# Optimization experiments

Hardware: AMD Instinct MI355X
Metric: run time of the kernel (lower is better)

Reference implementation:

```python
import jax, jax.numpy as jnp
import numpy as np

B, L, D, H, R = 2, 2048, 1024, 16, 512
HD = D // H  # head dim = 64
EPS = 1e-5


def layernorm(x, g, b):
    mu = jnp.mean(x, axis=-1, keepdims=True)
    var = jnp.mean(jnp.square(x - mu), axis=-1, keepdims=True)
    return (x - mu) * jax.lax.rsqrt(var + EPS) * g + b


def rel_pos_bias(res_pos, size):
    # Equivalent to the torch 'skew' causal_mask: bias[h, i, j] = res_pos[h, i-j]
    # if 0 <= i-j < R else -inf (causal + clipped relative distance).
    d = jnp.arange(size)[:, None] - jnp.arange(size)[None, :]  # (L, L)
    valid = (d >= 0) & (d < res_pos.shape[-1])
    gathered = res_pos[:, jnp.clip(d, 0, res_pos.shape[-1] - 1)]  # (H, L, L)
    return jnp.where(valid, gathered, -jnp.inf)


def setup_inputs() -> dict:
    key = jax.random.key(0)
    ks = jax.random.split(key, 12)
    s = lambda fan: 1.0 / np.sqrt(fan)
    return {
        "x": jax.random.normal(ks[0], (B, L, D), jnp.float32),
        "res_pos": jax.random.normal(ks[1], (H, R), jnp.float32) * 0.02,
        "w_qkv": jax.random.normal(ks[2], (D, 3 * D), jnp.float32) * s(D),
        "b_qkv": jnp.zeros((3 * D,), jnp.float32),
        "w_out": jax.random.normal(ks[3], (D, D), jnp.float32) * s(D),
        "b_out": jnp.zeros((D,), jnp.float32),
        "w1": jax.random.normal(ks[4], (D, 4 * D), jnp.float32) * s(D),
        "b1": jnp.zeros((4 * D,), jnp.float32),
        "w2": jax.random.normal(ks[5], (4 * D, D), jnp.float32) * s(4 * D),
        "b2": jnp.zeros((D,), jnp.float32),
        "ln1_g": jnp.ones((D,), jnp.float32),
        "ln1_b": jnp.zeros((D,), jnp.float32),
        "ln2_g": jnp.ones((D,), jnp.float32),
        "ln2_b": jnp.zeros((D,), jnp.float32),
    }


def reference(x, res_pos, w_qkv, b_qkv, w_out, b_out, w1, b1, w2, b2,
              ln1_g, ln1_b, ln2_g, ln2_b):
    b, l, _ = x.shape
    xn = layernorm(x, ln1_g, ln1_b)  # pre-norm
    qkv = xn @ w_qkv + b_qkv  # (B, L, 3D)
    q, k, v = jnp.split(qkv, 3, axis=-1)
    # (B, H, L, HD)
    q = q.reshape(b, l, H, HD).transpose(0, 2, 1, 3)
    k = k.reshape(b, l, H, HD).transpose(0, 2, 1, 3)
    v = v.reshape(b, l, H, HD).transpose(0, 2, 1, 3)
    scale = 1.0 / np.sqrt(HD)
    scores = jnp.einsum('bhqd,bhkd->bhqk', q, k) * scale
    scores = scores + rel_pos_bias(res_pos, l)[None]  # additive rel-pos causal mask
    attn = jax.nn.softmax(scores, axis=-1)
    ctx = jnp.einsum('bhqk,bhkd->bhqd', attn, v)
    ctx = ctx.transpose(0, 2, 1, 3).reshape(b, l, D)
    x = x + ctx @ w_out + b_out  # residual 1
    h = layernorm(x, ln2_g, ln2_b)
    h = jax.nn.relu(h @ w1 + b1) @ w2 + b2
    return x + h  # residual 2
```

## Files before the change

kernel.cpp:

```cpp
#include <hip/hip_runtime.h>
#include <math.h>

#define B_  2
#define L_  2048
#define D_  1024
#define H_  16
#define R_  512
#define HD_ 64
#define M_  (B_*L_)
#define EPS_ 1e-5f

typedef __attribute__((ext_vector_type(8))) short bf16x8;
typedef __attribute__((ext_vector_type(4))) float f32x4;

__device__ __forceinline__ unsigned short f2bf(float f) {
    unsigned int u = __float_as_uint(f);
    u += 0x7fffu + ((u >> 16) & 1u);
    return (unsigned short)(u >> 16);
}

__device__ __forceinline__ void gl2lds16(const void* g, void* l) {
    __builtin_amdgcn_global_load_lds(
        (const __attribute__((address_space(1))) unsigned int*)g,
        (__attribute__((address_space(3))) unsigned int*)l, 16, 0, 0);
}

__global__ __launch_bounds__(256) void prep_kernel(const float* __restrict__ w_qkv,
                                                   const float* __restrict__ w_out,
                                                   const float* __restrict__ w1,
                                                   const float* __restrict__ w2,
                                                   const float* __restrict__ x,
                                                   const float* __restrict__ ln1_g,
                                                   const float* __restrict__ ln1_b,
                                                   unsigned short* __restrict__ o_qkv,
                                                   unsigned short* __restrict__ o_out,
                                                   unsigned short* __restrict__ o_w1,
                                                   unsigned short* __restrict__ o_w2,
                                                   unsigned short* __restrict__ xn) {
    int id = blockIdx.x;
    int t = threadIdx.x;

    if (id >= 12288) {
        int row = id - 12288;
        const float4* xr = (const float4*)(x + (size_t)row * D_);
        float4 v = xr[t];
        float s  = v.x + v.y + v.z + v.w;
        float ss = v.x*v.x + v.y*v.y + v.z*v.z + v.w*v.w;
        #pragma unroll
        for (int o = 32; o > 0; o >>= 1) {
            s  += __shfl_down(s,  o);
            ss += __shfl_down(ss, o);
        }
        __shared__ float rs[4], rss[4];
        int wave = t >> 6, lane = t & 63;
        if (lane == 0) { rs[wave] = s; rss[wave] = ss; }
        __syncthreads();
        if (t == 0) {
            float a = 0.f, c = 0.f;
            for (int i = 0; i < 4; i++) { a += rs[i]; c += rss[i]; }
            rs[0] = a; rss[0] = c;
        }
        __syncthreads();
        float mean = rs[0] * (1.0f / D_);
        float var  = rss[0] * (1.0f / D_) - mean * mean;
        float inv  = rsqrtf(var + EPS_);
        float4 gv = ((const float4*)ln1_g)[t];
        float4 bv = ((const float4*)ln1_b)[t];
        ushort4 ob;
        ob.x = f2bf((v.x - mean) * inv * gv.x + bv.x);
        ob.y = f2bf((v.y - mean) * inv * gv.y + bv.y);
        ob.z = f2bf((v.z - mean) * inv * gv.z + bv.z);
        ob.w = f2bf((v.w - mean) * inv * gv.w + bv.w);
        ((ushort4*)(xn + (size_t)row * D_))[t] = ob;
        return;
    }

    const float* in; unsigned short* out; int K, N;
    if (id < 3072)      { in = w_qkv; out = o_qkv; K = 1024; N = 3072; }
    else if (id < 4096) { in = w_out; out = o_out; K = 1024; N = 1024; id -= 3072; }
    else if (id < 8192) { in = w1;    out = o_w1;  K = 1024; N = 4096; id -= 4096; }
    else                { in = w2;    out = o_w2;  K = 4096; N = 1024; id -= 8192; }
    int nb = N / 32;
    int bn = (id % nb) * 32, bk = (id / nb) * 32;

    __shared__ float tile[32][33];
    int r = t >> 3, c4 = (t & 7) * 4;
    float4 v = *(const float4*)(in + (size_t)(bk + r) * N + bn + c4);
    tile[r][c4+0] = v.x; tile[r][c4+1] = v.y; tile[r][c4+2] = v.z; tile[r][c4+3] = v.w;
    __syncthreads();
    ushort4 o;
    o.x = f2bf(tile[c4+0][r]);
    o.y = f2bf(tile[c4+1][r]);
    o.z = f2bf(tile[c4+2][r]);
    o.w = f2bf(tile[c4+3][r]);
    *(ushort4*)(out + (size_t)(bn + r) * K + bk + c4) = o;
}

__global__ __launch_bounds__(256) void ln_kernel(const float* __restrict__ x,
                                                 const float* __restrict__ g,
                                                 const float* __restrict__ b,
                                                 unsigned short* __restrict__ out) {
    int row = blockIdx.x;
    int t = threadIdx.x;
    const float4* xr = (const float4*)(x + (size_t)row * D_);
    float4 v = xr[t];
    float s  = v.x + v.y + v.z + v.w;
    float ss = v.x*v.x + v.y*v.y + v.z*v.z + v.w*v.w;
    #pragma unroll
    for (int o = 32; o > 0; o >>= 1) {
        s  += __shfl_down(s,  o);
        ss += __shfl_down(ss, o);
    }
    __shared__ float rs[4], rss[4];
    int wave = t >> 6, lane = t & 63;
    if (lane == 0) { rs[wave] = s; rss[wave] = ss; }
    __syncthreads();
    if (t == 0) {
        float a = 0.f, c = 0.f;
        for (int i = 0; i < 4; i++) { a += rs[i]; c += rss[i]; }
        rs[0] = a; rss[0] = c;
    }
    __syncthreads();
    float mean = rs[0] * (1.0f / D_);
    float var  = rss[0] * (1.0f / D_) - mean * mean;
    float inv  = rsqrtf(var + EPS_);
    float4 gv = ((const float4*)g)[t];
    float4 bv = ((const float4*)b)[t];
    ushort4 ob;
    ob.x = f2bf((v.x - mean) * inv * gv.x + bv.x);
    ob.y = f2bf((v.y - mean) * inv * gv.y + bv.y);
    ob.z = f2bf((v.z - mean) * inv * gv.z + bv.z);
    ob.w = f2bf((v.w - mean) * inv * gv.w + bv.w);
    ((ushort4*)(out + (size_t)row * D_))[t] = ob;
}

template<int BM, int KSPLIT, int RELU, int OUT_BF16>
__global__ __launch_bounds__(256) void gemm_mfma(const unsigned short* __restrict__ A,
                                                 const unsigned short* __restrict__ Wt,
                                                 const float* __restrict__ bias,
                                                 const float* __restrict__ res,
                                                 void* __restrict__ Cout,
                                                 int M, int N, int K) {
    constexpr int BN = 128;
    constexpr int BK = KSPLIT * 32;
    constexpr int TM = BM / 32;
    __shared__ __align__(16) unsigned short As[KSPLIT * BM * 32];
    __shared__ __align__(16) unsigned short Bs[KSPLIT * BN * 32];
    int t = threadIdx.x;
    int wave = t >> 6, lane = t & 63;
    int q = lane >> 4, cl = lane & 15;
    int bm = blockIdx.x * BM, bn = blockIdx.y * BN;
    int wm = (wave >> 1) * (BM / 2);
    int wn = (wave & 1) * 64;

    int sm  = t >> 2;
    int scx = t & 3;
    int ssrc = (scx ^ (sm & 3)) * 8;
    int sdst = scx * 8;

    int qa = (q ^ (cl & 3)) * 8;

    f32x4 acc[TM][4] = {};

    for (int kt = 0; kt < K; kt += BK) {
        __syncthreads();
        #pragma unroll
        for (int hh = 0; hh < KSPLIT; hh++) {
            #pragma unroll
            for (int s = 0; s < BM / 64; s++)
                gl2lds16(A + (size_t)(bm + s*64 + sm) * K + kt + hh*32 + ssrc,
                         &As[hh * BM * 32 + (s*64 + sm) * 32 + sdst]);
            #pragma unroll
            for (int s = 0; s < 2; s++)
                gl2lds16(Wt + (size_t)(bn + s*64 + sm) * K + kt + hh*32 + ssrc,
                         &Bs[hh * BN * 32 + (s*64 + sm) * 32 + sdst]);
        }
        __syncthreads();

        #pragma unroll
        for (int hh = 0; hh < KSPLIT; hh++) {
            bf16x8 af[TM], bfr[4];
            #pragma unroll
            for (int i = 0; i < TM; i++)
                af[i] = *(const bf16x8*)&As[hh * BM * 32 + (wm + i*16 + cl) * 32 + qa];
            #pragma unroll
            for (int j = 0; j < 4; j++)
                bfr[j] = *(const bf16x8*)&Bs[hh * BN * 32 + (wn + j*16 + cl) * 32 + qa];
            #pragma unroll
            for (int i = 0; i < TM; i++)
                #pragma unroll
                for (int j = 0; j < 4; j++)
                    acc[i][j] = __builtin_amdgcn_mfma_f32_16x16x32_bf16(
                                    af[i], bfr[j], acc[i][j], 0, 0, 0);
        }
    }

    #pragma unroll
    for (int i = 0; i < TM; i++) {
        #pragma unroll
        for (int j = 0; j < 4; j++) {
            #pragma unroll
            for (int r = 0; r < 4; r++) {
                int row = bm + wm + i*16 + q*4 + r;
                int col = bn + wn + j*16 + cl;
                float v = acc[i][j][r] + bias[col];
                if (RELU) v = fmaxf(v, 0.0f);
                if (res)  v += res[(size_t)row * N + col];
                if (OUT_BF16)
                    ((unsigned short*)Cout)[(size_t)row * N + col] = f2bf(v);
                else
                    ((float*)Cout)[(size_t)row * N + col] = v;
            }
        }
    }
}

#define AP_ 80
__global__ __launch_bounds__(256) void attn_mfma_kernel(const unsigned short* __restrict__ qkv,
                                                        const float* __restrict__ res_pos,
                                                        unsigned short* __restrict__ ctx) {
    int q0 = blockIdx.x * 128;
    int h  = blockIdx.y;
    int b  = blockIdx.z;
    int t  = threadIdx.x;
    int w  = t >> 6, lane = t & 63;
    int quad = lane >> 4, cl = lane & 15;

    __shared__ __align__(16) unsigned short sQP[128 * AP_];
    __shared__ __align__(16) unsigned short sK [64 * AP_];
    __shared__ __align__(16) unsigned short sVt[64 * AP_];
    __shared__ float sBias[R_];

    const int bL = b * L_;
    const unsigned short* base = qkv + (size_t)bL * 3072;

    #pragma unroll
    for (int c = t; c < 1024; c += 256) {
        int row = c >> 3, off = (c & 7) * 8;
        uint4 v = *(const uint4*)(base + (size_t)(q0 + row) * 3072 + h * HD_ + off);
        *(uint4*)&sQP[row * AP_ + off] = v;
    }
    sBias[t]       = res_pos[h * R_ + t]       - 20.0f;
    sBias[t + 256] = res_pos[h * R_ + t + 256] - 20.0f;
    __syncthreads();

    bf16x8 qf[2][2];
    #pragma unroll
    for (int i = 0; i < 2; i++) {
        qf[i][0] = *(const bf16x8*)&sQP[(w*32 + i*16 + cl) * AP_ + quad*8];
        qf[i][1] = *(const bf16x8*)&sQP[(w*32 + i*16 + cl) * AP_ + 32 + quad*8];
    }

    f32x4 accO[2][4] = {};
    float l_r[2][4] = {};

    int klo = q0 - (R_ - 1); if (klo < 0) klo = 0;
    int kt0 = klo & ~63;
    const float scale = 0.125f;

    for (int k0 = kt0; k0 <= q0 + 64; k0 += 64) {
        __syncthreads();
        #pragma unroll
        for (int c = t; c < 512; c += 256) {
            int row = c >> 3, off = (c & 7) * 8;
            uint4 v = *(const uint4*)(base + (size_t)(k0 + row) * 3072 + D_ + h * HD_ + off);
            *(uint4*)&sK[row * AP_ + off] = v;
        }
        {
            int c2 = t & 31, dg = t >> 5;
            int cl_ = c2 & 15, jb = (c2 >> 4) * 2;
            int ka = jb * 16 + cl_;
            const unsigned short* va = base + (size_t)(k0 + ka) * 3072 + 2*D_ + h * HD_ + dg*8;
            uint4 a4 = *(const uint4*)va;
            uint4 b4 = *(const uint4*)(va + (size_t)16 * 3072);
            const unsigned short* pa = (const unsigned short*)&a4;
            const unsigned short* pb = (const unsigned short*)&b4;
            #pragma unroll
            for (int i = 0; i < 8; i++) {
                unsigned int packed = (unsigned int)pa[i] | ((unsigned int)pb[i] << 16);
                *(unsigned int*)&sVt[(dg*8 + i) * AP_ + 4*cl_ + jb] = packed;
            }
        }
        __syncthreads();

        f32x4 sacc[2][4] = {};
        #pragma unroll
        for (int j = 0; j < 4; j++) {
            bf16x8 kf0 = *(const bf16x8*)&sK[(j*16 + cl) * AP_ + quad*8];
            bf16x8 kf1 = *(const bf16x8*)&sK[(j*16 + cl) * AP_ + 32 + quad*8];
            #pragma unroll
            for (int i = 0; i < 2; i++) {
                sacc[i][j] = __builtin_amdgcn_mfma_f32_16x16x32_bf16(qf[i][0], kf0, sacc[i][j], 0, 0, 0);
                sacc[i][j] = __builtin_amdgcn_mfma_f32_16x16x32_bf16(qf[i][1], kf1, sacc[i][j], 0, 0, 0);
            }
        }

        #pragma unroll
        for (int i = 0; i < 2; i++) {
            #pragma unroll
            for (int r = 0; r < 4; r++) {
                int qrow = q0 + w*32 + i*16 + quad*4 + r;
                unsigned short pk[4];
                float lacc = 0.f;
                #pragma unroll
                for (int j = 0; j < 4; j++) {
                    int key = k0 + j*16 + cl;
                    int diff = qrow - key;
                    bool valid = ((unsigned)diff) < (unsigned)R_;
                    int dc = valid ? diff : 0;
                    float p = valid ? __expf(fmaf(sacc[i][j][r], scale, sBias[dc])) : 0.f;
                    lacc += p;
                    pk[j] = f2bf(p);
                }
                l_r[i][r] += lacc;
                unsigned int lo = (unsigned int)pk[0] | ((unsigned int)pk[1] << 16);
                unsigned int hi = (unsigned int)pk[2] | ((unsigned int)pk[3] << 16);
                uint2 pv; pv.x = lo; pv.y = hi;
                *(uint2*)&sQP[(w*32 + i*16 + quad*4 + r) * AP_ + 4*cl] = pv;
            }
        }
        __syncthreads();

        bf16x8 pf[2][2];
        #pragma unroll
        for (int i = 0; i < 2; i++) {
            pf[i][0] = *(const bf16x8*)&sQP[(w*32 + i*16 + cl) * AP_ + quad*8];
            pf[i][1] = *(const bf16x8*)&sQP[(w*32 + i*16 + cl) * AP_ + 32 + quad*8];
        }
        #pragma unroll
        for (int j = 0; j < 4; j++) {
            bf16x8 vf0 = *(const bf16x8*)&sVt[(j*16 + cl) * AP_ + quad*8];
            bf16x8 vf1 = *(const bf16x8*)&sVt[(j*16 + cl) * AP_ + 32 + quad*8];
            #pragma unroll
            for (int i = 0; i < 2; i++) {
                accO[i][j] = __builtin_amdgcn_mfma_f32_16x16x32_bf16(pf[i][0], vf0, accO[i][j], 0, 0, 0);
                accO[i][j] = __builtin_amdgcn_mfma_f32_16x16x32_bf16(pf[i][1], vf1, accO[i][j], 0, 0, 0);
            }
        }
    }

    #pragma unroll
    for (int i = 0; i < 2; i++) {
        #pragma unroll
        for (int r = 0; r < 4; r++) {
            float l = l_r[i][r];
            #pragma unroll
            for (int o = 8; o > 0; o >>= 1) l += __shfl_xor(l, o);
            float inv = 1.0f / l;
            int row = bL + q0 + w*32 + i*16 + quad*4 + r;
            #pragma unroll
            for (int j = 0; j < 4; j++)
                ctx[(size_t)row * D_ + h * HD_ + j*16 + cl] = f2bf(accO[i][j][r] * inv);
        }
    }
}

extern "C" void kernel_launch(void* const* d_in, const int* in_sizes, int n_in,
                              void* d_out, int out_size, void* d_ws, size_t ws_size,
                              hipStream_t stream) {
    const float* x      = (const float*)d_in[0];
    const float* res_pos= (const float*)d_in[1];
    const float* w_qkv  = (const float*)d_in[2];
    const float* b_qkv  = (const float*)d_in[3];
    const float* w_out  = (const float*)d_in[4];
    const float* b_out  = (const float*)d_in[5];
    const float* w1     = (const float*)d_in[6];
    const float* b1     = (const float*)d_in[7];
    const float* w2     = (const float*)d_in[8];
    const float* b2     = (const float*)d_in[9];
    const float* ln1_g  = (const float*)d_in[10];
    const float* ln1_b  = (const float*)d_in[11];
    const float* ln2_g  = (const float*)d_in[12];
    const float* ln2_b  = (const float*)d_in[13];
    float* out = (float*)d_out;
    char* ws = (char*)d_ws;

    unsigned short* act_bf = (unsigned short*)ws;
    unsigned short* wqkvT  = (unsigned short*)(ws + ((size_t)8  << 20));
    unsigned short* woutT  = (unsigned short*)(ws + ((size_t)14 << 20));
    unsigned short* w1T    = (unsigned short*)(ws + ((size_t)16 << 20));
    unsigned short* w2T    = (unsigned short*)(ws + ((size_t)24 << 20));
    unsigned short* qkv_bf = (unsigned short*)(ws + ((size_t)32 << 20));
    unsigned short* h1_bf  = (unsigned short*)(ws + ((size_t)32 << 20));

    prep_kernel<<<16384, 256, 0, stream>>>(w_qkv, w_out, w1, w2,
                                           x, ln1_g, ln1_b,
                                           wqkvT, woutT, w1T, w2T, act_bf);
    gemm_mfma<64,2,0,1><<<dim3(M_/64, 3072/128), 256, 0, stream>>>(
        act_bf, wqkvT, b_qkv, nullptr, qkv_bf, M_, 3072, 1024);
    attn_mfma_kernel<<<dim3(L_/128, H_, B_), 256, 0, stream>>>(qkv_bf, res_pos, act_bf);
    gemm_mfma<64,4,0,0><<<dim3(M_/64, 1024/128), 256, 0, stream>>>(
        act_bf, woutT, b_out, x, out, M_, 1024, 1024);
    ln_kernel<<<M_, 256, 0, stream>>>(out, ln2_g, ln2_b, act_bf);
    gemm_mfma<64,2,1,1><<<dim3(M_/64, 4096/128), 256, 0, stream>>>(
        act_bf, w1T, b1, nullptr, h1_bf, M_, 4096, 1024);
    gemm_mfma<64,4,0,0><<<dim3(M_/64, 1024/128), 256, 0, stream>>>(
        h1_bf, w2T, b2, out, out, M_, 1024, 4096);
}
```

Baseline: 349.3 us.

## Fuse all stages into one persistent kernel with software grid barriers

New measurement: 712.9 us. 104% more time.

```diff
diff --git a/kernel.cpp b/kernel.cpp
--- a/kernel.cpp
+++ b/kernel.cpp
@@ -9,6 +9,8 @@
 #define HD_ 64
 #define M_  (B_*L_)
 #define EPS_ 1e-5f
+#define GRID_ 512
+#define MAGIC_ 0x13572468u
 
 typedef __attribute__((ext_vector_type(8))) short bf16x8;
 typedef __attribute__((ext_vector_type(4))) float f32x4;
@@ -25,24 +27,336 @@
         (__attribute__((address_space(3))) unsigned int*)l, 16, 0, 0);
 }
 
-__global__ __launch_bounds__(256) void prep_kernel(const float* __restrict__ w_qkv,
-                                                   const float* __restrict__ w_out,
-                                                   const float* __restrict__ w1,
-                                                   const float* __restrict__ w2,
-                                                   const float* __restrict__ x,
-                                                   const float* __restrict__ ln1_g,
-                                                   const float* __restrict__ ln1_b,
-                                                   unsigned short* __restrict__ o_qkv,
-                                                   unsigned short* __restrict__ o_out,
-                                                   unsigned short* __restrict__ o_w1,
-                                                   unsigned short* __restrict__ o_w2,
-                                                   unsigned short* __restrict__ xn) {
-    int id = blockIdx.x;
+__device__ __forceinline__ void grid_barrier(unsigned* bar, int blk) {
+    __syncthreads();
+    if (threadIdx.x == 0) {
+        while (__hip_atomic_load(&bar[0], __ATOMIC_ACQUIRE, __HIP_MEMORY_SCOPE_AGENT) != MAGIC_)
+            __builtin_amdgcn_s_sleep(2);
+        unsigned g0 = __hip_atomic_load(&bar[1], __ATOMIC_RELAXED, __HIP_MEMORY_SCOPE_AGENT);
+        int grp = blk >> 3;
+        unsigned a = __hip_atomic_fetch_add(&bar[16 + grp*16], 1u,
+                        __ATOMIC_ACQ_REL, __HIP_MEMORY_SCOPE_AGENT);
+        if (a == 7u) {
+            __hip_atomic_store(&bar[16 + grp*16], 0u, __ATOMIC_RELAXED, __HIP_MEMORY_SCOPE_AGENT);
+            unsigned a2 = __hip_atomic_fetch_add(&bar[2], 1u,
+                            __ATOMIC_ACQ_REL, __HIP_MEMORY_SCOPE_AGENT);
+            if (a2 == 63u) {
+                __hip_atomic_store(&bar[2], 0u, __ATOMIC_RELAXED, __HIP_MEMORY_SCOPE_AGENT);
+                __hip_atomic_fetch_add(&bar[1], 1u, __ATOMIC_RELEASE, __HIP_MEMORY_SCOPE_AGENT);
+            }
+        }
+        while (__hip_atomic_load(&bar[1], __ATOMIC_ACQUIRE, __HIP_MEMORY_SCOPE_AGENT) == g0)
+            __builtin_amdgcn_s_sleep(2);
+    }
+    __syncthreads();
+}
+
+__device__ __forceinline__ void gemm_tile(const unsigned short* __restrict__ A,
+                                          const unsigned short* __restrict__ Wt,
+                                          const float* __restrict__ bias,
+                                          const float* __restrict__ res,
+                                          void* __restrict__ Cout,
+                                          int bm, int bn, int N, int K,
+                                          bool relu, bool out_bf16,
+                                          unsigned short* As, unsigned short* Bs) {
     int t = threadIdx.x;
-
-    if (id >= 12288) {
-        int row = id - 12288;
-        const float4* xr = (const float4*)(x + (size_t)row * D_);
+    int wave = t >> 6, lane = t & 63;
+    int q = lane >> 4, cl = lane & 15;
+    int wm = (wave >> 1) * 32;
+    int wn = (wave & 1) * 64;
+
+    int sm  = t >> 2;
+    int scx = t & 3;
+    int ssrc = (scx ^ (sm & 3)) * 8;
+    int sdst = scx * 8;
+    int qa = (q ^ (cl & 3)) * 8;
+
+    f32x4 acc[2][4] = {};
+
+    for (int kt = 0; kt < K; kt += 128) {
+        __syncthreads();
+        #pragma unroll
+        for (int hh = 0; hh < 4; hh++) {
+            gl2lds16(A + (size_t)(bm + sm) * K + kt + hh*32 + ssrc,
+                     &As[hh * 64 * 32 + sm * 32 + sdst]);
+            #pragma unroll
+            for (int s = 0; s < 2; s++)
+                gl2lds16(Wt + (size_t)(bn + s*64 + sm) * K + kt + hh*32 + ssrc,
+                         &Bs[hh * 128 * 32 + (s*64 + sm) * 32 + sdst]);
+        }
+        __syncthreads();
+
+        #pragma unroll
+        for (int hh = 0; hh < 4; hh++) {
+            bf16x8 af[2], bfr[4];
+            #pragma unroll
+            for (int i = 0; i < 2; i++)
+                af[i] = *(const bf16x8*)&As[hh * 64 * 32 + (wm + i*16 + cl) * 32 + qa];
+            #pragma unroll
+            for (int j = 0; j < 4; j++)
+                bfr[j] = *(const bf16x8*)&Bs[hh * 128 * 32 + (wn + j*16 + cl) * 32 + qa];
+            #pragma unroll
+            for (int i = 0; i < 2; i++)
+                #pragma unroll
+                for (int j = 0; j < 4; j++)
+                    acc[i][j] = __builtin_amdgcn_mfma_f32_16x16x32_bf16(
+                                    af[i], bfr[j], acc[i][j], 0, 0, 0);
+        }
+    }
+
+    #pragma unroll
+    for (int i = 0; i < 2; i++) {
+        #pragma unroll
+        for (int j = 0; j < 4; j++) {
+            #pragma unroll
+            for (int r = 0; r < 4; r++) {
+                int row = bm + wm + i*16 + q*4 + r;
+                int col = bn + wn + j*16 + cl;
+                float v = acc[i][j][r] + bias[col];
+                if (relu) v = fmaxf(v, 0.0f);
+                if (res)  v += res[(size_t)row * N + col];
+                if (out_bf16)
+                    ((unsigned short*)Cout)[(size_t)row * N + col] = f2bf(v);
+                else
+                    ((float*)Cout)[(size_t)row * N + col] = v;
+            }
+        }
+    }
+}
+
+struct MegaParams {
+    const float *x, *res_pos;
+    const float *b_qkv, *b_out, *b1, *b2;
+    const float *w_qkv, *w_out, *w1, *w2;
+    const float *ln1_g, *ln1_b, *ln2_g, *ln2_b;
+    float* out;
+    unsigned short *act_bf, *wqkvT, *woutT, *w1T, *w2T, *qkv_bf, *h1_bf;
+    unsigned* bar;
+};
+
+#define AP_ 80
+__global__ __launch_bounds__(256, 2) void mega_kernel(MegaParams p) {
+    __shared__ __align__(16) unsigned short smem[24576];
+    int blk = blockIdx.x;
+    int t   = threadIdx.x;
+    int wave = t >> 6, lane = t & 63;
+    int quad = lane >> 4, cl = lane & 15;
+
+    unsigned short* As = smem;
+    unsigned short* Bs = smem + 8192;
+
+    if (blk == 0 && t == 0) {
+        p.bar[1] = 0; p.bar[2] = 0;
+        for (int g = 0; g < 64; g++) p.bar[16 + g*16] = 0;
+        __hip_atomic_store(&p.bar[0], MAGIC_, __ATOMIC_RELEASE, __HIP_MEMORY_SCOPE_AGENT);
+    }
+
+    for (int id0 = blk; id0 < 16384; id0 += GRID_) {
+        __syncthreads();
+        if (id0 >= 12288) {
+            int row = id0 - 12288;
+            float* red = (float*)smem;
+            const float4* xr = (const float4*)(p.x + (size_t)row * D_);
+            float4 v = xr[t];
+            float s  = v.x + v.y + v.z + v.w;
+            float ss = v.x*v.x + v.y*v.y + v.z*v.z + v.w*v.w;
+            #pragma unroll
+            for (int o = 32; o > 0; o >>= 1) {
+                s  += __shfl_down(s,  o);
+                ss += __shfl_down(ss, o);
+            }
+            if (lane == 0) { red[wave] = s; red[4 + wave] = ss; }
+            __syncthreads();
+            if (t == 0) {
+                float a = 0.f, c = 0.f;
+                for (int i = 0; i < 4; i++) { a += red[i]; c += red[4 + i]; }
+                red[0] = a; red[4] = c;
+            }
+            __syncthreads();
+            float mean = red[0] * (1.0f / D_);
+            float var  = red[4] * (1.0f / D_) - mean * mean;
+            float inv  = rsqrtf(var + EPS_);
+            float4 gv = ((const float4*)p.ln1_g)[t];
+            float4 bv = ((const float4*)p.ln1_b)[t];
+            ushort4 ob;
+            ob.x = f2bf((v.x - mean) * inv * gv.x + bv.x);
+            ob.y = f2bf((v.y - mean) * inv * gv.y + bv.y);
+            ob.z = f2bf((v.z - mean) * inv * gv.z + bv.z);
+            ob.w = f2bf((v.w - mean) * inv * gv.w + bv.w);
+            ((ushort4*)(p.act_bf + (size_t)row * D_))[t] = ob;
+        } else {
+            int id = id0;
+            const float* in; unsigned short* outw; int K, N;
+            if (id < 3072)      { in = p.w_qkv; outw = p.wqkvT; K = 1024; N = 3072; }
+            else if (id < 4096) { in = p.w_out; outw = p.woutT; K = 1024; N = 1024; id -= 3072; }
+            else if (id < 8192) { in = p.w1;    outw = p.w1T;   K = 1024; N = 4096; id -= 4096; }
+            else                { in = p.w2;    outw = p.w2T;   K = 4096; N = 1024; id -= 8192; }
+            int nb = N / 32;
+            int bn = (id % nb) * 32, bk = (id / nb) * 32;
+            float* tile = (float*)smem;
+            int r = t >> 3, c4 = (t & 7) * 4;
+            float4 v = *(const float4*)(in + (size_t)(bk + r) * N + bn + c4);
+            tile[r*33 + c4+0] = v.x; tile[r*33 + c4+1] = v.y;
+            tile[r*33 + c4+2] = v.z; tile[r*33 + c4+3] = v.w;
+            __syncthreads();
+            ushort4 o;
+            o.x = f2bf(tile[(c4+0)*33 + r]);
+            o.y = f2bf(tile[(c4+1)*33 + r]);
+            o.z = f2bf(tile[(c4+2)*33 + r]);
+            o.w = f2bf(tile[(c4+3)*33 + r]);
+            *(ushort4*)(outw + (size_t)(bn + r) * K + bk + c4) = o;
+        }
+    }
+    grid_barrier(p.bar, blk);
+
+    for (int idx = blk; idx < 64 * 24; idx += GRID_)
+        gemm_tile(p.act_bf, p.wqkvT, p.b_qkv, nullptr, p.qkv_bf,
+                  (idx & 63) * 64, (idx >> 6) * 128, 3072, 1024, false, true, As, Bs);
+    grid_barrier(p.bar, blk);
+
+    {
+        int q0 = (blk & 15) * 128;
+        int h  = (blk >> 4) & 15;
+        int b  = blk >> 8;
+        unsigned short* sQP = smem;
+        unsigned short* sK  = smem + 10240;
+        unsigned short* sVt = smem + 15360;
+        float* sBias        = (float*)(smem + 20480);
+
+        const int bL = b * L_;
+        const unsigned short* base = p.qkv_bf + (size_t)bL * 3072;
+
+        __syncthreads();
+        #pragma unroll
+        for (int c = t; c < 1024; c += 256) {
+            int row = c >> 3, off = (c & 7) * 8;
+            uint4 v = *(const uint4*)(base + (size_t)(q0 + row) * 3072 + h * HD_ + off);
+            *(uint4*)&sQP[row * AP_ + off] = v;
+        }
+        sBias[t]       = p.res_pos[h * R_ + t]       - 20.0f;
+        sBias[t + 256] = p.res_pos[h * R_ + t + 256] - 20.0f;
+        __syncthreads();
+
+        bf16x8 qf[2][2];
+        #pragma unroll
+        for (int i = 0; i < 2; i++) {
+            qf[i][0] = *(const bf16x8*)&sQP[(wave*32 + i*16 + cl) * AP_ + quad*8];
+            qf[i][1] = *(const bf16x8*)&sQP[(wave*32 + i*16 + cl) * AP_ + 32 + quad*8];
+        }
+
+        f32x4 accO[2][4] = {};
+        float l_r[2][4] = {};
+
+        int klo = q0 - (R_ - 1); if (klo < 0) klo = 0;
+        int kt0 = klo & ~63;
+        const float scale = 0.125f;
+
+        for (int k0 = kt0; k0 <= q0 + 64; k0 += 64) {
+            __syncthreads();
+            #pragma unroll
+            for (int c = t; c < 512; c += 256) {
+                int row = c >> 3, off = (c & 7) * 8;
+                uint4 v = *(const uint4*)(base + (size_t)(k0 + row) * 3072 + D_ + h * HD_ + off);
+                *(uint4*)&sK[row * AP_ + off] = v;
+            }
+            {
+                int c2 = t & 31, dg = t >> 5;
+                int cl_ = c2 & 15, jb = (c2 >> 4) * 2;
+                int ka = jb * 16 + cl_;
+                const unsigned short* va = base + (size_t)(k0 + ka) * 3072 + 2*D_ + h * HD_ + dg*8;
+                uint4 a4 = *(const uint4*)va;
+                uint4 b4 = *(const uint4*)(va + (size_t)16 * 3072);
+                const unsigned short* pa = (const unsigned short*)&a4;
+                const unsigned short* pb = (const unsigned short*)&b4;
+                #pragma unroll
+                for (int i = 0; i < 8; i++) {
+                    unsigned int packed = (unsigned int)pa[i] | ((unsigned int)pb[i] << 16);
+                    *(unsigned int*)&sVt[(dg*8 + i) * AP_ + 4*cl_ + jb] = packed;
+                }
+            }
+            __syncthreads();
+
+            f32x4 sacc[2][4] = {};
+            #pragma unroll
+            for (int j = 0; j < 4; j++) {
+                bf16x8 kf0 = *(const bf16x8*)&sK[(j*16 + cl) * AP_ + quad*8];
+                bf16x8 kf1 = *(const bf16x8*)&sK[(j*16 + cl) * AP_ + 32 + quad*8];
+                #pragma unroll
+                for (int i = 0; i < 2; i++) {
+                    sacc[i][j] = __builtin_amdgcn_mfma_f32_16x16x32_bf16(qf[i][0], kf0, sacc[i][j], 0, 0, 0);
+                    sacc[i][j] = __builtin_amdgcn_mfma_f32_16x16x32_bf16(qf[i][1], kf1, sacc[i][j], 0, 0, 0);
+                }
+            }
+
+            #pragma unroll
+            for (int i = 0; i < 2; i++) {
+                #pragma unroll
+                for (int r = 0; r < 4; r++) {
+                    int qrow = q0 + wave*32 + i*16 + quad*4 + r;
+                    unsigned short pk[4];
+                    float lacc = 0.f;
+                    #pragma unroll
+                    for (int j = 0; j < 4; j++) {
+                        int key = k0 + j*16 + cl;
+                        int diff = qrow - key;
+                        bool valid = ((unsigned)diff) < (unsigned)R_;
+                        int dc = valid ? diff : 0;
+                        float pv = valid ? __expf(fmaf(sacc[i][j][r], scale, sBias[dc])) : 0.f;
+                        lacc += pv;
+                        pk[j] = f2bf(pv);
+                    }
+                    l_r[i][r] += lacc;
+                    unsigned int lo = (unsigned int)pk[0] | ((unsigned int)pk[1] << 16);
+                    unsigned int hi = (unsigned int)pk[2] | ((unsigned int)pk[3] << 16);
+                    uint2 pv2; pv2.x = lo; pv2.y = hi;
+                    *(uint2*)&sQP[(wave*32 + i*16 + quad*4 + r) * AP_ + 4*cl] = pv2;
+                }
+            }
+            __syncthreads();
+
+            bf16x8 pf[2][2];
+            #pragma unroll
+            for (int i = 0; i < 2; i++) {
+                pf[i][0] = *(const bf16x8*)&sQP[(wave*32 + i*16 + cl) * AP_ + quad*8];
+                pf[i][1] = *(const bf16x8*)&sQP[(wave*32 + i*16 + cl) * AP_ + 32 + quad*8];
+            }
+            #pragma unroll
+            for (int j = 0; j < 4; j++) {
+                bf16x8 vf0 = *(const bf16x8*)&sVt[(j*16 + cl) * AP_ + quad*8];
+                bf16x8 vf1 = *(const bf16x8*)&sVt[(j*16 + cl) * AP_ + 32 + quad*8];
+                #pragma unroll
+                for (int i = 0; i < 2; i++) {
+                    accO[i][j] = __builtin_amdgcn_mfma_f32_16x16x32_bf16(pf[i][0], vf0, accO[i][j], 0, 0, 0);
+                    accO[i][j] = __builtin_amdgcn_mfma_f32_16x16x32_bf16(pf[i][1], vf1, accO[i][j], 0, 0, 0);
+                }
+            }
+        }
+
+        #pragma unroll
+        for (int i = 0; i < 2; i++) {
+            #pragma unroll
+            for (int r = 0; r < 4; r++) {
+                float l = l_r[i][r];
+                #pragma unroll
+                for (int o = 8; o > 0; o >>= 1) l += __shfl_xor(l, o);
+                float inv = 1.0f / l;
+                int row = bL + q0 + wave*32 + i*16 + quad*4 + r;
+                #pragma unroll
+                for (int j = 0; j < 4; j++)
+                    p.act_bf[(size_t)row * D_ + h * HD_ + j*16 + cl] = f2bf(accO[i][j][r] * inv);
+            }
+        }
+    }
+    grid_barrier(p.bar, blk);
+
+    gemm_tile(p.act_bf, p.woutT, p.b_out, p.x, p.out,
+              (blk & 63) * 64, (blk >> 6) * 128, 1024, 1024, false, false, As, Bs);
+    grid_barrier(p.bar, blk);
+
+    for (int row = blk; row < M_; row += GRID_) {
+        __syncthreads();
+        float* red = (float*)smem;
+        const float4* xr = (const float4*)(p.out + (size_t)row * D_);
         float4 v = xr[t];
         float s  = v.x + v.y + v.z + v.w;
         float ss = v.x*v.x + v.y*v.y + v.z*v.z + v.w*v.w;
@@ -51,349 +365,65 @@
             s  += __shfl_down(s,  o);
             ss += __shfl_down(ss, o);
         }
-        __shared__ float rs[4], rss[4];
-        int wave = t >> 6, lane = t & 63;
-        if (lane == 0) { rs[wave] = s; rss[wave] = ss; }
+        if (lane == 0) { red[wave] = s; red[4 + wave] = ss; }
         __syncthreads();
         if (t == 0) {
             float a = 0.f, c = 0.f;
-            for (int i = 0; i < 4; i++) { a += rs[i]; c += rss[i]; }
-            rs[0] = a; rss[0] = c;
-        }
-        __syncthreads();
-        float mean = rs[0] * (1.0f / D_);
-        float var  = rss[0] * (1.0f / D_) - mean * mean;
+            for (int i = 0; i < 4; i++) { a += red[i]; c += red[4 + i]; }
+            red[0] = a; red[4] = c;
+        }
+        __syncthreads();
+        float mean = red[0] * (1.0f / D_);
+        float var  = red[4] * (1.0f / D_) - mean * mean;
         float inv  = rsqrtf(var + EPS_);
-        float4 gv = ((const float4*)ln1_g)[t];
-        float4 bv = ((const float4*)ln1_b)[t];
+        float4 gv = ((const float4*)p.ln2_g)[t];
+        float4 bv = ((const float4*)p.ln2_b)[t];
         ushort4 ob;
         ob.x = f2bf((v.x - mean) * inv * gv.x + bv.x);
         ob.y = f2bf((v.y - mean) * inv * gv.y + bv.y);
         ob.z = f2bf((v.z - mean) * inv * gv.z + bv.z);
         ob.w = f2bf((v.w - mean) * inv * gv.w + bv.w);
-        ((ushort4*)(xn + (size_t)row * D_))[t] = ob;
-        return;
-    }
-
-    const float* in; unsigned short* out; int K, N;
-    if (id < 3072)      { in = w_qkv; out = o_qkv; K = 1024; N = 3072; }
-    else if (id < 4096) { in = w_out; out = o_out; K = 1024; N = 1024; id -= 3072; }
-    else if (id < 8192) { in = w1;    out = o_w1;  K = 1024; N = 4096; id -= 4096; }
-    else                { in = w2;    out = o_w2;  K = 4096; N = 1024; id -= 8192; }
-    int nb = N / 32;
-    int bn = (id % nb) * 32, bk = (id / nb) * 32;
-
-    __shared__ float tile[32][33];
-    int r = t >> 3, c4 = (t & 7) * 4;
-    float4 v = *(const float4*)(in + (size_t)(bk + r) * N + bn + c4);
-    tile[r][c4+0] = v.x; tile[r][c4+1] = v.y; tile[r][c4+2] = v.z; tile[r][c4+3] = v.w;
-    __syncthreads();
-    ushort4 o;
-    o.x = f2bf(tile[c4+0][r]);
-    o.y = f2bf(tile[c4+1][r]);
-    o.z = f2bf(tile[c4+2][r]);
-    o.w = f2bf(tile[c4+3][r]);
-    *(ushort4*)(out + (size_t)(bn + r) * K + bk + c4) = o;
-}
-
-__global__ __launch_bounds__(256) void ln_kernel(const float* __restrict__ x,
-                                                 const float* __restrict__ g,
-                                                 const float* __restrict__ b,
-                                                 unsigned short* __restrict__ out) {
-    int row = blockIdx.x;
-    int t = threadIdx.x;
-    const float4* xr = (const float4*)(x + (size_t)row * D_);
-    float4 v = xr[t];
-    float s  = v.x + v.y + v.z + v.w;
-    float ss = v.x*v.x + v.y*v.y + v.z*v.z + v.w*v.w;
-    #pragma unroll
-    for (int o = 32; o > 0; o >>= 1) {
-        s  += __shfl_down(s,  o);
-        ss += __shfl_down(ss, o);
-    }
-    __shared__ float rs[4], rss[4];
-    int wave = t >> 6, lane = t & 63;
-    if (lane == 0) { rs[wave] = s; rss[wave] = ss; }
-    __syncthreads();
-    if (t == 0) {
-        float a = 0.f, c = 0.f;
-        for (int i = 0; i < 4; i++) { a += rs[i]; c += rss[i]; }
-        rs[0] = a; rss[0] = c;
-    }
-    __syncthreads();
-    float mean = rs[0] * (1.0f / D_);
-    float var  = rss[0] * (1.0f / D_) - mean * mean;
-    float inv  = rsqrtf(var + EPS_);
-    float4 gv = ((const float4*)g)[t];
-    float4 bv = ((const float4*)b)[t];
-    ushort4 ob;
-    ob.x = f2bf((v.x - mean) * inv * gv.x + bv.x);
-    ob.y = f2bf((v.y - mean) * inv * gv.y + bv.y);
-    ob.z = f2bf((v.z - mean) * inv * gv.z + bv.z);
-    ob.w = f2bf((v.w - mean) * inv * gv.w + bv.w);
-    ((ushort4*)(out + (size_t)row * D_))[t] = ob;
-}
-
-template<int BM, int KSPLIT, int RELU, int OUT_BF16>
-__global__ __launch_bounds__(256) void gemm_mfma(const unsigned short* __restrict__ A,
-                                                 const unsigned short* __restrict__ Wt,
-                                                 const float* __restrict__ bias,
-                                                 const float* __restrict__ res,
-                                                 void* __restrict__ Cout,
-                                                 int M, int N, int K) {
-    constexpr int BN = 128;
-    constexpr int BK = KSPLIT * 32;
-    constexpr int TM = BM / 32;
-    __shared__ __align__(16) unsigned short As[KSPLIT * BM * 32];
-    __shared__ __align__(16) unsigned short Bs[KSPLIT * BN * 32];
-    int t = threadIdx.x;
-    int wave = t >> 6, lane = t & 63;
-    int q = lane >> 4, cl = lane & 15;
-    int bm = blockIdx.x * BM, bn = blockIdx.y * BN;
-    int wm = (wave >> 1) * (BM / 2);
-    int wn = (wave & 1) * 64;
-
-    int sm  = t >> 2;
-    int scx = t & 3;
-    int ssrc = (scx ^ (sm & 3)) * 8;
-    int sdst = scx * 8;
-
-    int qa = (q ^ (cl & 3)) * 8;
-
-    f32x4 acc[TM][4] = {};
-
-    for (int kt = 0; kt < K; kt += BK) {
-        __syncthreads();
-        #pragma unroll
-        for (int hh = 0; hh < KSPLIT; hh++) {
-            #pragma unroll
-            for (int s = 0; s < BM / 64; s++)
-                gl2lds16(A + (size_t)(bm + s*64 + sm) * K + kt + hh*32 + ssrc,
-                         &As[hh * BM * 32 + (s*64 + sm) * 32 + sdst]);
-            #pragma unroll
-            for (int s = 0; s < 2; s++)
-                gl2lds16(Wt + (size_t)(bn + s*64 + sm) * K + kt + hh*32 + ssrc,
-                         &Bs[hh * BN * 32 + (s*64 + sm) * 32 + sdst]);
-        }
-        __syncthreads();
-
-        #pragma unroll
-        for (int hh = 0; hh < KSPLIT; hh++) {
-            bf16x8 af[TM], bfr[4];
-            #pragma unroll
-            for (int i = 0; i < TM; i++)
-                af[i] = *(const bf16x8*)&As[hh * BM * 32 + (wm + i*16 + cl) * 32 + qa];
-            #pragma unroll
-            for (int j = 0; j < 4; j++)
-                bfr[j] = *(const bf16x8*)&Bs[hh * BN * 32 + (wn + j*16 + cl) * 32 + qa];
-            #pragma unroll
-            for (int i = 0; i < TM; i++)
-                #pragma unroll
-                for (int j = 0; j < 4; j++)
-                    acc[i][j] = __builtin_amdgcn_mfma_f32_16x16x32_bf16(
-                                    af[i], bfr[j], acc[i][j], 0, 0, 0);
-        }
-    }
-
-    #pragma unroll
-    for (int i = 0; i < TM; i++) {
-        #pragma unroll
-        for (int j = 0; j < 4; j++) {
-            #pragma unroll
-            for (int r = 0; r < 4; r++) {
-                int row = bm + wm + i*16 + q*4 + r;
-                int col = bn + wn + j*16 + cl;
-                float v = acc[i][j][r] + bias[col];
-                if (RELU) v = fmaxf(v, 0.0f);
-                if (res)  v += res[(size_t)row * N + col];
-                if (OUT_BF16)
-                    ((unsigned short*)Cout)[(size_t)row * N + col] = f2bf(v);
-                else
-                    ((float*)Cout)[(size_t)row * N + col] = v;
-            }
-        }
-    }
-}
-
-#define AP_ 80
-__global__ __launch_bounds__(256) void attn_mfma_kernel(const unsigned short* __restrict__ qkv,
-                                                        const float* __restrict__ res_pos,
-                                                        unsigned short* __restrict__ ctx) {
-    int q0 = blockIdx.x * 128;
-    int h  = blockIdx.y;
-    int b  = blockIdx.z;
-    int t  = threadIdx.x;
-    int w  = t >> 6, lane = t & 63;
-    int quad = lane >> 4, cl = lane & 15;
-
-    __shared__ __align__(16) unsigned short sQP[128 * AP_];
-    __shared__ __align__(16) unsigned short sK [64 * AP_];
-    __shared__ __align__(16) unsigned short sVt[64 * AP_];
-    __shared__ float sBias[R_];
-
-    const int bL = b * L_;
-    const unsigned short* base = qkv + (size_t)bL * 3072;
-
-    #pragma unroll
-    for (int c = t; c < 1024; c += 256) {
-        int row = c >> 3, off = (c & 7) * 8;
-        uint4 v = *(const uint4*)(base + (size_t)(q0 + row) * 3072 + h * HD_ + off);
-        *(uint4*)&sQP[row * AP_ + off] = v;
-    }
-    sBias[t]       = res_pos[h * R_ + t]       - 20.0f;
-    sBias[t + 256] = res_pos[h * R_ + t + 256] - 20.0f;
-    __syncthreads();
-
-    bf16x8 qf[2][2];
-    #pragma unroll
-    for (int i = 0; i < 2; i++) {
-        qf[i][0] = *(const bf16x8*)&sQP[(w*32 + i*16 + cl) * AP_ + quad*8];
-        qf[i][1] = *(const bf16x8*)&sQP[(w*32 + i*16 + cl) * AP_ + 32 + quad*8];
-    }
-
-    f32x4 accO[2][4] = {};
-    float l_r[2][4] = {};
-
-    int klo = q0 - (R_ - 1); if (klo < 0) klo = 0;
-    int kt0 = klo & ~63;
-    const float scale = 0.125f;
-
-    for (int k0 = kt0; k0 <= q0 + 64; k0 += 64) {
-        __syncthreads();
-        #pragma unroll
-        for (int c = t; c < 512; c += 256) {
-            int row = c >> 3, off = (c & 7) * 8;
-            uint4 v = *(const uint4*)(base + (size_t)(k0 + row) * 3072 + D_ + h * HD_ + off);
-            *(uint4*)&sK[row * AP_ + off] = v;
-        }
-        {
-            int c2 = t & 31, dg = t >> 5;
-            int cl_ = c2 & 15, jb = (c2 >> 4) * 2;
-            int ka = jb * 16 + cl_;
-            const unsigned short* va = base + (size_t)(k0 + ka) * 3072 + 2*D_ + h * HD_ + dg*8;
-            uint4 a4 = *(const uint4*)va;
-            uint4 b4 = *(const uint4*)(va + (size_t)16 * 3072);
-            const unsigned short* pa = (const unsigned short*)&a4;
-            const unsigned short* pb = (const unsigned short*)&b4;
-            #pragma unroll
-            for (int i = 0; i < 8; i++) {
-                unsigned int packed = (unsigned int)pa[i] | ((unsigned int)pb[i] << 16);
-                *(unsigned int*)&sVt[(dg*8 + i) * AP_ + 4*cl_ + jb] = packed;
-            }
-        }
-        __syncthreads();
-
-        f32x4 sacc[2][4] = {};
-        #pragma unroll
-        for (int j = 0; j < 4; j++) {
-            bf16x8 kf0 = *(const bf16x8*)&sK[(j*16 + cl) * AP_ + quad*8];
-            bf16x8 kf1 = *(const bf16x8*)&sK[(j*16 + cl) * AP_ + 32 + quad*8];
-            #pragma unroll
-            for (int i = 0; i < 2; i++) {
-                sacc[i][j] = __builtin_amdgcn_mfma_f32_16x16x32_bf16(qf[i][0], kf0, sacc[i][j], 0, 0, 0);
-                sacc[i][j] = __builtin_amdgcn_mfma_f32_16x16x32_bf16(qf[i][1], kf1, sacc[i][j], 0, 0, 0);
-            }
-        }
-
-        #pragma unroll
-        for (int i = 0; i < 2; i++) {
-            #pragma unroll
-            for (int r = 0; r < 4; r++) {
-                int qrow = q0 + w*32 + i*16 + quad*4 + r;
-                unsigned short pk[4];
-                float lacc = 0.f;
-                #pragma unroll
-                for (int j = 0; j < 4; j++) {
-                    int key = k0 + j*16 + cl;
-                    int diff = qrow - key;
-                    bool valid = ((unsigned)diff) < (unsigned)R_;
-                    int dc = valid ? diff : 0;
-                    float p = valid ? __expf(fmaf(sacc[i][j][r], scale, sBias[dc])) : 0.f;
-                    lacc += p;
-                    pk[j] = f2bf(p);
-                }
-                l_r[i][r] += lacc;
-                unsigned int lo = (unsigned int)pk[0] | ((unsigned int)pk[1] << 16);
-                unsigned int hi = (unsigned int)pk[2] | ((unsigned int)pk[3] << 16);
-                uint2 pv; pv.x = lo; pv.y = hi;
-                *(uint2*)&sQP[(w*32 + i*16 + quad*4 + r) * AP_ + 4*cl] = pv;
-            }
-        }
-        __syncthreads();
-
-        bf16x8 pf[2][2];
-        #pragma unroll
-        for (int i = 0; i < 2; i++) {
-            pf[i][0] = *(const bf16x8*)&sQP[(w*32 + i*16 + cl) * AP_ + quad*8];
-            pf[i][1] = *(const bf16x8*)&sQP[(w*32 + i*16 + cl) * AP_ + 32 + quad*8];
-        }
-        #pragma unroll
-        for (int j = 0; j < 4; j++) {
-            bf16x8 vf0 = *(const bf16x8*)&sVt[(j*16 + cl) * AP_ + quad*8];
-            bf16x8 vf1 = *(const bf16x8*)&sVt[(j*16 + cl) * AP_ + 32 + quad*8];
-            #pragma unroll
-            for (int i = 0; i < 2; i++) {
-                accO[i][j] = __builtin_amdgcn_mfma_f32_16x16x32_bf16(pf[i][0], vf0, accO[i][j], 0, 0, 0);
-                accO[i][j] = __builtin_amdgcn_mfma_f32_16x16x32_bf16(pf[i][1], vf1, accO[i][j], 0, 0, 0);
-            }
-        }
-    }
-
-    #pragma unroll
-    for (int i = 0; i < 2; i++) {
-        #pragma unroll
-        for (int r = 0; r < 4; r++) {
-            float l = l_r[i][r];
-            #pragma unroll
-            for (int o = 8; o > 0; o >>= 1) l += __shfl_xor(l, o);
-            float inv = 1.0f / l;
-            int row = bL + q0 + w*32 + i*16 + quad*4 + r;
-            #pragma unroll
-            for (int j = 0; j < 4; j++)
-                ctx[(size_t)row * D_ + h * HD_ + j*16 + cl] = f2bf(accO[i][j][r] * inv);
-        }
-    }
+        ((ushort4*)(p.act_bf + (size_t)row * D_))[t] = ob;
+    }
+    grid_barrier(p.bar, blk);
+
+    for (int idx = blk; idx < 64 * 32; idx += GRID_)
+        gemm_tile(p.act_bf, p.w1T, p.b1, nullptr, p.h1_bf,
+                  (idx & 63) * 64, (idx >> 6) * 128, 4096, 1024, true, true, As, Bs);
+    grid_barrier(p.bar, blk);
+
+    gemm_tile(p.h1_bf, p.w2T, p.b2, p.out, p.out,
+              (blk & 63) * 64, (blk >> 6) * 128, 1024, 4096, false, false, As, Bs);
 }
 
 extern "C" void kernel_launch(void* const* d_in, const int* in_sizes, int n_in,
                               void* d_out, int out_size, void* d_ws, size_t ws_size,
                               hipStream_t stream) {
-    const float* x      = (const float*)d_in[0];
-    const float* res_pos= (const float*)d_in[1];
-    const float* w_qkv  = (const float*)d_in[2];
-    const float* b_qkv  = (const float*)d_in[3];
-    const float* w_out  = (const float*)d_in[4];
-    const float* b_out  = (const float*)d_in[5];
-    const float* w1     = (const float*)d_in[6];
-    const float* b1     = (const float*)d_in[7];
-    const float* w2     = (const float*)d_in[8];
-    const float* b2     = (const float*)d_in[9];
-    const float* ln1_g  = (const float*)d_in[10];
-    const float* ln1_b  = (const float*)d_in[11];
-    const float* ln2_g  = (const float*)d_in[12];
-    const float* ln2_b  = (const float*)d_in[13];
-    float* out = (float*)d_out;
     char* ws = (char*)d_ws;
-
-    unsigned short* act_bf = (unsigned short*)ws;
-    unsigned short* wqkvT  = (unsigned short*)(ws + ((size_t)8  << 20));
-    unsigned short* woutT  = (unsigned short*)(ws + ((size_t)14 << 20));
-    unsigned short* w1T    = (unsigned short*)(ws + ((size_t)16 << 20));
-    unsigned short* w2T    = (unsigned short*)(ws + ((size_t)24 << 20));
-    unsigned short* qkv_bf = (unsigned short*)(ws + ((size_t)32 << 20));
-    unsigned short* h1_bf  = (unsigned short*)(ws + ((size_t)32 << 20));
-
-    prep_kernel<<<16384, 256, 0, stream>>>(w_qkv, w_out, w1, w2,
-                                           x, ln1_g, ln1_b,
-                                           wqkvT, woutT, w1T, w2T, act_bf);
-    gemm_mfma<64,2,0,1><<<dim3(M_/64, 3072/128), 256, 0, stream>>>(
-        act_bf, wqkvT, b_qkv, nullptr, qkv_bf, M_, 3072, 1024);
-    attn_mfma_kernel<<<dim3(L_/128, H_, B_), 256, 0, stream>>>(qkv_bf, res_pos, act_bf);
-    gemm_mfma<64,4,0,0><<<dim3(M_/64, 1024/128), 256, 0, stream>>>(
-        act_bf, woutT, b_out, x, out, M_, 1024, 1024);
-    ln_kernel<<<M_, 256, 0, stream>>>(out, ln2_g, ln2_b, act_bf);
-    gemm_mfma<64,2,1,1><<<dim3(M_/64, 4096/128), 256, 0, stream>>>(
-        act_bf, w1T, b1, nullptr, h1_bf, M_, 4096, 1024);
-    gemm_mfma<64,4,0,0><<<dim3(M_/64, 1024/128), 256, 0, stream>>>(
-        h1_bf, w2T, b2, out, out, M_, 1024, 4096);
-}
+    MegaParams p;
+    p.x      = (const float*)d_in[0];
+    p.res_pos= (const float*)d_in[1];
+    p.w_qkv  = (const float*)d_in[2];
+    p.b_qkv  = (const float*)d_in[3];
+    p.w_out  = (const float*)d_in[4];
+    p.b_out  = (const float*)d_in[5];
+    p.w1     = (const float*)d_in[6];
+    p.b1     = (const float*)d_in[7];
+    p.w2     = (const float*)d_in[8];
+    p.b2     = (const float*)d_in[9];
+    p.ln1_g  = (const float*)d_in[10];
+    p.ln1_b  = (const float*)d_in[11];
+    p.ln2_g  = (const float*)d_in[12];
+    p.ln2_b  = (const float*)d_in[13];
+    p.out    = (float*)d_out;
+    p.act_bf = (unsigned short*)ws;
+    p.wqkvT  = (unsigned short*)(ws + ((size_t)8  << 20));
+    p.woutT  = (unsigned short*)(ws + ((size_t)14 << 20));
+    p.w1T    = (unsigned short*)(ws + ((size_t)16 << 20));
+    p.w2T    = (unsigned short*)(ws + ((size_t)24 << 20));
+    p.qkv_bf = (unsigned short*)(ws + ((size_t)32 << 20));
+    p.h1_bf  = (unsigned short*)(ws + ((size_t)32 << 20));
+    p.bar    = (unsigned*)(ws + ((size_t)72 << 20));
+
+    mega_kernel<<<GRID_, 256, 0, stream>>>(p);
+}
```
